# Kernel optimization log

Hardware: AMD Instinct MI355X
Metric: run time of the kernel (lower is better)

Reference implementation:

```python
import jax, jax.numpy as jnp
import numpy as np

D = 256          # input_dim
H = 4            # num_heads
W = 4            # window_size
NUM_SCALES = 3
FRACTAL = 2
NUM_CLASSES = 7


def _pool(t, ksize):
    # reflect-pad along time by ksize//2 each side, then avg_pool1d(kernel=stride=ksize)
    p = ksize // 2
    t = jnp.pad(t, ((0, 0), (p, p), (0, 0)), mode='reflect')
    B, Tp, F = t.shape
    L = Tp // ksize
    return t[:, :L * ksize].reshape(B, L, ksize, F).mean(axis=2)


def _window_attn(q, k, v):
    # windowed multi-head self-attention with zero-pad to a multiple of W
    B, T, F = q.shape
    pad = (-T) % W
    if pad:
        q = jnp.pad(q, ((0, 0), (0, pad), (0, 0)))
        k = jnp.pad(k, ((0, 0), (0, pad), (0, 0)))
        v = jnp.pad(v, ((0, 0), (0, pad), (0, 0)))
    Tp = T + pad
    nw = Tp // W
    hd = F // H
    scale = 1.0 / np.sqrt(hd).astype(np.float32)
    # [B, nw, W, H, hd] -> [B, nw, H, W, hd]
    qh = q.reshape(B, nw, W, H, hd).transpose(0, 1, 3, 2, 4)
    kh = k.reshape(B, nw, W, H, hd).transpose(0, 1, 3, 2, 4)
    vh = v.reshape(B, nw, W, H, hd).transpose(0, 1, 3, 2, 4)
    attn = jnp.einsum('bnhqd,bnhkd->bnhqk', qh, kh) * scale
    attn = jax.nn.softmax(attn, axis=-1)
    out = jnp.einsum('bnhqk,bnhkd->bnhqd', attn, vh)
    out = out.transpose(0, 1, 3, 2, 4).reshape(B, Tp, F)
    return out[:, :T]


def _upsample_nearest(f, out_len):
    # matches torch F.interpolate(mode='nearest'): src = floor(i * in / out)
    in_len = f.shape[1]
    idx = jnp.minimum((jnp.arange(out_len) * in_len) // out_len, in_len - 1)
    return f[:, idx]


def setup_inputs() -> dict:
    key = jax.random.key(0)
    ks = jax.random.split(key, 14)
    s = 1.0 / np.sqrt(D).astype(np.float32)
    inp = {
        'x': jax.random.normal(ks[0], (32, 4096, D), dtype=jnp.float32),
        'Wq': jax.random.normal(ks[1], (D, D), dtype=jnp.float32) * s,
        'bq': jnp.zeros((D,), jnp.float32),
        'Wk': jax.random.normal(ks[2], (D, D), dtype=jnp.float32) * s,
        'bk': jnp.zeros((D,), jnp.float32),
        'Wv': jax.random.normal(ks[3], (D, D), dtype=jnp.float32) * s,
        'bv': jnp.zeros((D,), jnp.float32),
        'Wp': jax.random.normal(ks[4], (D, D), dtype=jnp.float32) * s,
        'bp': jnp.zeros((D,), jnp.float32),
        'Wc1': jax.random.normal(ks[5], (D, D), dtype=jnp.float32) * s,
        'bc1': jnp.zeros((D,), jnp.float32),
        'Wc2': jax.random.normal(ks[6], (D, NUM_CLASSES), dtype=jnp.float32) * s,
        'bc2': jnp.zeros((NUM_CLASSES,), jnp.float32),
    }
    return inp


def reference(x, Wq, bq, Wk, bk, Wv, bv, Wp, bp, Wc1, bc1, Wc2, bc2):
    B, T, F = x.shape
    q = x @ Wq + bq
    k = x @ Wk + bk
    v = x @ Wv + bv
    # multi-scale temporal operator + per-scale fractal windowed attention
    outs = []
    for s_idx in range(1, NUM_SCALES + 1):
        ksize = FRACTAL ** (s_idx - 1)
        if ksize == 1:
            qs, ks_, vs = q, k, v
        else:
            qs, ks_, vs = _pool(q, ksize), _pool(k, ksize), _pool(v, ksize)
        outs.append(_window_attn(qs, ks_, vs))
    # scale mixer: nearest upsample + exact GELU + sum + proj
    summed = sum(jax.nn.gelu(_upsample_nearest(f, T), approximate=False) for f in outs)
    fused = summed @ Wp + bp
    # classifier (dropout inactive in eval)
    h = fused.mean(axis=1)
    h = jax.nn.relu(h @ Wc1 + bc1)
    logits = h @ Wc2 + bc2
    return logits
```

## Files before the change

kernel.cpp:

```cpp
#include <hip/hip_runtime.h>

#define DD 256
#define TT 4096
#define BB 32

typedef __attribute__((ext_vector_type(8))) short short8;
typedef __attribute__((ext_vector_type(4))) float floatx4;

__device__ __forceinline__ unsigned short f2bf(float f) {
    unsigned u = __builtin_bit_cast(unsigned, f);
    unsigned r = u + 0x7FFFu + ((u >> 16) & 1u);
    return (unsigned short)(r >> 16);
}
__device__ __forceinline__ float bf2f(unsigned short h) {
    return __builtin_bit_cast(float, (unsigned)h << 16);
}
__device__ __forceinline__ float2 unpk(unsigned u) {
    float2 r;
    r.x = __builtin_bit_cast(float, u << 16);
    r.y = __builtin_bit_cast(float, u & 0xFFFF0000u);
    return r;
}

#define GLDS16(g, l)                                                        \
    __builtin_amdgcn_global_load_lds(                                       \
        (const __attribute__((address_space(1))) void*)(g),                 \
        (__attribute__((address_space(3))) void*)(l), 16, 0, 0)

__global__ __launch_bounds__(256)
void prep_x_kernel(const float* __restrict__ X, unsigned short* __restrict__ Xp)
{
    size_t i = ((size_t)blockIdx.x * 256 + threadIdx.x) * 8;
    float4 a = *(const float4*)(X + i);
    float4 b = *(const float4*)(X + i + 4);
    short8 o;
    o[0] = (short)f2bf(a.x); o[1] = (short)f2bf(a.y);
    o[2] = (short)f2bf(a.z); o[3] = (short)f2bf(a.w);
    o[4] = (short)f2bf(b.x); o[5] = (short)f2bf(b.y);
    o[6] = (short)f2bf(b.z); o[7] = (short)f2bf(b.w);
    size_t row = i >> 8;
    int k = (int)(i & 255);
    size_t off = (size_t)(k >> 5) * (131072u * 32u) + row * 32 + (k & 31);
    *(short8*)(Xp + off) = o;
}

__global__ void prep_w_kernel(const float* __restrict__ Wq,
                              const float* __restrict__ Wk,
                              const float* __restrict__ Wv,
                              unsigned short* __restrict__ Wt)
{
    const int z = blockIdx.y;
    const int k = blockIdx.x;
    const int n = threadIdx.x;
    const float* W = (z == 0) ? Wq : (z == 1) ? Wk : Wv;
    float w = W[k * 256 + n];
    unsigned short hi = f2bf(w);
    unsigned short lo = f2bf(w - bf2f(hi));
    size_t base = (size_t)z * 131072;
    size_t off = (size_t)(k >> 5) * 8192 + (size_t)n * 32 + (k & 31);
    Wt[base +         off] = hi;
    Wt[base + 65536 + off] = lo;
}

__global__ __launch_bounds__(256, 3)
void qkv_mfma_kernel(const unsigned short* __restrict__ Xp,
                     const unsigned short* __restrict__ Wt,
                     const float* __restrict__ bq, const float* __restrict__ bk,
                     const float* __restrict__ bv,
                     unsigned short* __restrict__ Q, unsigned short* __restrict__ Kp,
                     unsigned short* __restrict__ V)
{
    const int z = blockIdx.z;
    const unsigned short* Wz = Wt + (size_t)z * 131072;
    const float* bias = (z == 0) ? bq : (z == 1) ? bk : bv;
    unsigned short* Y = (z == 0) ? Q : (z == 1) ? Kp : V;

    __shared__ __align__(16) unsigned char smem[49152];

    const int tid = threadIdx.x;
    const int lane = tid & 63, wave = tid >> 6;
    const int wm = wave & 1, wn = wave >> 1;
    const int l15 = lane & 15, lq = lane >> 4;
    const int col0 = blockIdx.x * 128;
    const size_t row0 = (size_t)blockIdx.y * 128;

    floatx4 acc[4][4];
    #pragma unroll
    for (int i = 0; i < 4; ++i)
        #pragma unroll
        for (int j = 0; j < 4; ++j)
            acc[i][j] = (floatx4){0.f, 0.f, 0.f, 0.f};

    auto stage = [&](int p, int pb) {
        unsigned short* As = (unsigned short*)(smem + pb * 8192);
        unsigned short* Bs = (unsigned short*)(smem + 16384 + pb * 16384);
        const unsigned short* Ap = Xp + (size_t)p * (131072u * 32u);
        const unsigned short* Bp = Wz + (size_t)p * 8192;
        #pragma unroll
        for (int it = 0; it < 2; ++it) {
            int flat = it * 256 + tid;
            int m = flat >> 2, c = flat & 3;
            int sc = c ^ ((m >> 1) & 3);
            GLDS16(Ap + (row0 + m) * 32 + sc * 8, As + flat * 8);
        }
        #pragma unroll
        for (int half = 0; half < 2; ++half)
            #pragma unroll
            for (int it = 0; it < 2; ++it) {
                int flat = it * 256 + tid;
                int n = flat >> 2, c = flat & 3;
                int sc = c ^ ((n >> 1) & 3);
                GLDS16(Bp + half * 65536 + (size_t)(col0 + n) * 32 + sc * 8,
                       Bs + half * 4096 + flat * 8);
            }
    };

    stage(0, 0);
    __syncthreads();

    for (int k = 0; k < 8; ++k) {
        const int pb = k & 1;
        if (k < 7) stage(k + 1, pb ^ 1);

        const unsigned short* As = (const unsigned short*)(smem + pb * 8192);
        const unsigned short* Bs = (const unsigned short*)(smem + 16384 + pb * 16384);

        short8 a[4];
        #pragma unroll
        for (int mt = 0; mt < 4; ++mt) {
            int row = wm * 64 + mt * 16 + l15;
            a[mt] = *(const short8*)(As + row * 32 + (lq ^ ((row >> 1) & 3)) * 8);
        }
        #pragma unroll
        for (int nt = 0; nt < 4; ++nt) {
            int nr = wn * 64 + nt * 16 + l15;
            const unsigned short* bp = Bs + nr * 32 + (lq ^ ((nr >> 1) & 3)) * 8;
            short8 bh = *(const short8*)bp;
            short8 bl = *(const short8*)(bp + 4096);
            #pragma unroll
            for (int mt = 0; mt < 4; ++mt) {
                acc[mt][nt] = __builtin_amdgcn_mfma_f32_16x16x32_bf16(a[mt], bh, acc[mt][nt], 0, 0, 0);
                acc[mt][nt] = __builtin_amdgcn_mfma_f32_16x16x32_bf16(a[mt], bl, acc[mt][nt], 0, 0, 0);
            }
        }
        __syncthreads();
    }

    unsigned short* Cs = (unsigned short*)(smem + wave * 8192);
    #pragma unroll
    for (int nt = 0; nt < 4; ++nt) {
        float bv_ = bias[col0 + wn * 64 + nt * 16 + l15];
        #pragma unroll
        for (int mt = 0; mt < 4; ++mt)
            #pragma unroll
            for (int r = 0; r < 4; ++r) {
                int row = mt * 16 + lq * 4 + r;
                Cs[row * 64 + nt * 16 + l15] = f2bf(acc[mt][nt][r] + bv_);
            }
    }
    #pragma unroll
    for (int p = 0; p < 8; ++p) {
        int row = p * 8 + (lane >> 3);
        float4 d = *(const float4*)(Cs + row * 64 + (lane & 7) * 8);
        *(float4*)(Y + (row0 + wm * 64 + row) * 256 + col0 + wn * 64 + (lane & 7) * 8) = d;
    }
}

__device__ __forceinline__ float gelu2(float x) {
    float z = fabsf(x) * 0.70710678118654752f;
    float t = __builtin_amdgcn_rcpf(fmaf(z, 0.3275911f, 1.0f));
    float p = fmaf(t, 1.061405429f, -1.453152027f);
    p = fmaf(p, t, 1.421413741f);
    p = fmaf(p, t, -0.284496736f);
    p = fmaf(p, t, 0.254829592f);
    p = p * t;
    float e = __expf(-z * z);
    float erf_abs = fmaf(-p, e, 1.0f);
    float erfv = copysignf(erf_abs, x);
    return x * (1.0f + erfv);
}
__device__ __forceinline__ void addu4(uint4 d, float* f) {
    float2 t;
    t = unpk(d.x); f[0] += t.x; f[1] += t.y;
    t = unpk(d.y); f[2] += t.x; f[3] += t.y;
    t = unpk(d.z); f[4] += t.x; f[5] += t.y;
    t = unpk(d.w); f[6] += t.x; f[7] += t.y;
}

#define SPAN 32
#define NROW 34

template<int KS>
__device__ __forceinline__ void pool_qk(const unsigned short* __restrict__ qb,
                                        const unsigned short* __restrict__ kb,
                                        int rp,
                                        float* __restrict__ qf,
                                        float* __restrict__ kf)
{
    #pragma unroll
    for (int j = 0; j < KS; ++j) {
        int ra = (rp >> (8 * j)) & 0xFF;
        uint4 qd = *(const uint4*)(qb + ra * 256);
        uint4 kd = *(const uint4*)(kb + ra * 256);
        addu4(qd, qf);
        addu4(kd, kf);
    }
}

template<int KS>
__device__ __forceinline__ void pool_v(const unsigned short* __restrict__ vb,
                                       int rp, float* __restrict__ vf)
{
    #pragma unroll
    for (int j = 0; j < KS; ++j) {
        int ra = (rp >> (8 * j)) & 0xFF;
        uint4 vd = *(const uint4*)(vb + ra * 256);
        addu4(vd, vf);
    }
}

__global__ __launch_bounds__(256, 3)
void attn_fused_kernel(const unsigned short* __restrict__ Q,
                       const unsigned short* __restrict__ K,
                       const unsigned short* __restrict__ V,
                       float* __restrict__ acc)
{
    __shared__ __align__(16) unsigned char smem[3 * NROW * 256 * 2];
    unsigned short* qkvs = (unsigned short*)smem;
    float* scratch = (float*)smem;

    const int tid = threadIdx.x;
    const int s = blockIdx.x;
    const int b = blockIdx.y;
    const int r0 = s * SPAN;
    const int rbase = r0 - 2;

    #pragma unroll
    for (int t = 0; t < 3; ++t) {
        const unsigned short* src =
            ((t == 0) ? Q : (t == 1) ? K : V) + (size_t)b * TT * DD;
        #pragma unroll
        for (int it = 0; it < 5; ++it) {
            int flat = it * 256 + tid;
            if (flat < NROW * 32) {
                int row = flat >> 5, dc = flat & 31;
                int g = rbase + row;
                g = (g < 0) ? 0 : g;
                int c = (((dc >> 2) & 3) << 3) | ((dc & 3) << 1) | ((dc >> 4) & 1);
                GLDS16(src + (size_t)g * DD + c * 8,
                       qkvs + t * (NROW * 256) + flat * 8);
            }
        }
    }
    __syncthreads();

    const int slot = tid >> 2, lq = tid & 3;
    const int head = slot & 3, u = slot >> 2;
    int ksize, LEN, w; bool active = true;
    if (u < 8)       { ksize = 1; LEN = 4096; w = s * 8 + u; }
    else if (u < 12) { ksize = 2; LEN = 2049; w = s * 4 + (u - 8); }
    else if (u < 14) { ksize = 4; LEN = 1025; w = s * 2 + (u - 12); }
    else if (u == 14){ ksize = 2; LEN = 2049; w = 512; active = (s == 127); }
    else             { ksize = 4; LEN = 1025; w = 256; active = (s == 127); }

    const int f0 = head * 64 + lq * 16;
    const int fperm = head * 32 + lq * 8;

    float accL[16];
    #pragma unroll
    for (int e = 0; e < 16; ++e) accL[e] = 0.f;

    if (active) {
        int rp[4]; float cwh[4]; int vmask = 0;
        for (int i = 0; i < 4; ++i) {
            int p = w * 4 + i;
            bool vv = (p < LEN);
            if (vv) vmask |= (1 << i);
            int pc = vv ? p : 0;
            int r[4] = {0, 0, 0, 0};
            if (ksize == 1) { r[0] = pc; }
            else if (ksize == 2) {
                if (pc == 0)            { r[0] = 0;      r[1] = 1;      }
                else if (pc == LEN - 1) { r[0] = TT - 2; r[1] = TT - 1; }
                else                    { r[0] = 2 * pc - 1; r[1] = 2 * pc; }
            } else {
                if (pc == 0)            { r[0] = 2; r[1] = 1; r[2] = 0; r[3] = 1; }
                else if (pc == LEN - 1) { r[0] = TT - 3; r[1] = TT - 2; r[2] = TT - 2; r[3] = TT - 1; }
                else                    { r[0] = 4*pc - 2; r[1] = 4*pc - 1; r[2] = 4*pc; r[3] = 4*pc + 1; }
            }
            int rr = 0;
            #pragma unroll
            for (int j = 0; j < 4; ++j) rr |= ((r[j] - rbase) & 0xFF) << (8 * j);
            rp[i] = rr;
            float c = 0.5f;
            if (ksize == 2)
                c = 0.5f * (float)(((p + 1) * TT + 2048) / 2049 - (p * TT + 2048) / 2049);
            else if (ksize == 4)
                c = 0.5f * (float)(((p + 1) * TT + 1024) / 1025 - (p * TT + 1024) / 1025);
            cwh[i] = vv ? c : 0.f;
        }
        const float inv_k = 1.0f / (float)ksize;
        const float sscale = 0.125f * inv_k * inv_k;

        float S[4][4];
        #pragma unroll
        for (int i = 0; i < 4; ++i)
            #pragma unroll
            for (int j = 0; j < 4; ++j) S[i][j] = 0.f;

        for (int half = 0; half < 2; ++half) {
            float qf[4][8], kf[4][8];
            const unsigned short* qb = qkvs + half * 128 + fperm;
            const unsigned short* kb = qb + NROW * 256;
            #pragma unroll
            for (int i = 0; i < 4; ++i) {
                #pragma unroll
                for (int e = 0; e < 8; ++e) { qf[i][e] = 0.f; kf[i][e] = 0.f; }
                if (vmask & (1 << i)) {
                    if (ksize == 1)      pool_qk<1>(qb, kb, rp[i], qf[i], kf[i]);
                    else if (ksize == 2) pool_qk<2>(qb, kb, rp[i], qf[i], kf[i]);
                    else                 pool_qk<4>(qb, kb, rp[i], qf[i], kf[i]);
                }
            }
            #pragma unroll
            for (int i = 0; i < 4; ++i)
                #pragma unroll
                for (int j = 0; j < 4; ++j) {
                    float d = 0.f;
                    #pragma unroll
                    for (int e = 0; e < 8; ++e) d = fmaf(qf[i][e], kf[j][e], d);
                    S[i][j] += d;
                }
        }
        #pragma unroll
        for (int i = 0; i < 4; ++i)
            #pragma unroll
            for (int j = 0; j < 4; ++j) {
                float t = S[i][j];
                t += __shfl_xor(t, 1, 64);
                t += __shfl_xor(t, 2, 64);
                S[i][j] = t * sscale;
            }
        float P[4][4];
        #pragma unroll
        for (int i = 0; i < 4; ++i) {
            float m = fmaxf(fmaxf(S[i][0], S[i][1]), fmaxf(S[i][2], S[i][3]));
            float e0 = __expf(S[i][0] - m), e1 = __expf(S[i][1] - m);
            float e2 = __expf(S[i][2] - m), e3 = __expf(S[i][3] - m);
            float inv = inv_k * __builtin_amdgcn_rcpf(e0 + e1 + e2 + e3);
            P[i][0] = e0 * inv; P[i][1] = e1 * inv; P[i][2] = e2 * inv; P[i][3] = e3 * inv;
        }

        for (int half = 0; half < 2; ++half) {
            float vf[4][8];
            const unsigned short* vb = qkvs + 2 * NROW * 256 + half * 128 + fperm;
            #pragma unroll
            for (int i = 0; i < 4; ++i) {
                #pragma unroll
                for (int e = 0; e < 8; ++e) vf[i][e] = 0.f;
                if (vmask & (1 << i)) {
                    if (ksize == 1)      pool_v<1>(vb, rp[i], vf[i]);
                    else if (ksize == 2) pool_v<2>(vb, rp[i], vf[i]);
                    else                 pool_v<4>(vb, rp[i], vf[i]);
                }
            }
            #pragma unroll
            for (int i = 0; i < 4; ++i) {
                if (!(vmask & (1 << i))) continue;
                #pragma unroll
                for (int e = 0; e < 8; ++e) {
                    float o = P[i][0]*vf[0][e] + P[i][1]*vf[1][e]
                            + P[i][2]*vf[2][e] + P[i][3]*vf[3][e];
                    accL[half * 8 + e] += cwh[i] * gelu2(o);
                }
            }
        }
    }

    __syncthreads();
    #pragma unroll
    for (int e = 0; e < 16; e += 4) {
        float4 d = {accL[e], accL[e+1], accL[e+2], accL[e+3]};
        *(float4*)(scratch + u * 256 + f0 + e) = d;
    }
    __syncthreads();
    float sum = 0.f;
    #pragma unroll
    for (int uu = 0; uu < 16; ++uu) sum += scratch[uu * 256 + tid];
    atomicAdd(&acc[b * DD + tid], sum);
}

__global__ __launch_bounds__(256)
void classifier_kernel(const float* __restrict__ acc,
                       const float* __restrict__ Wp,  const float* __restrict__ bp,
                       const float* __restrict__ Wc1, const float* __restrict__ bc1,
                       const float* __restrict__ Wc2, const float* __restrict__ bc2,
                       float* __restrict__ out)
{
    const int b = blockIdx.x;
    const int d = threadIdx.x;
    __shared__ float sm[256], sf[256], sh[256];

    sm[d] = acc[b * 256 + d] * (1.0f / 4096.0f);
    __syncthreads();

    float s = bp[d];
    for (int kk = 0; kk < 256; ++kk) s = fmaf(sm[kk], Wp[kk * 256 + d], s);
    sf[d] = s;
    __syncthreads();

    s = bc1[d];
    for (int kk = 0; kk < 256; ++kk) s = fmaf(sf[kk], Wc1[kk * 256 + d], s);
    sh[d] = fmaxf(s, 0.0f);
    __syncthreads();

    if (d < 7) {
        s = bc2[d];
        for (int kk = 0; kk < 256; ++kk) s = fmaf(sh[kk], Wc2[kk * 7 + d], s);
        out[b * 7 + d] = s;
    }
}

extern "C" void kernel_launch(void* const* d_in, const int* in_sizes, int n_in,
                              void* d_out, int out_size, void* d_ws, size_t ws_size,
                              hipStream_t stream)
{
    const float* x   = (const float*)d_in[0];
    const float* Wq  = (const float*)d_in[1];
    const float* bq  = (const float*)d_in[2];
    const float* Wk  = (const float*)d_in[3];
    const float* bk  = (const float*)d_in[4];
    const float* Wv  = (const float*)d_in[5];
    const float* bv  = (const float*)d_in[6];
    const float* Wp  = (const float*)d_in[7];
    const float* bp  = (const float*)d_in[8];
    const float* Wc1 = (const float*)d_in[9];
    const float* bc1 = (const float*)d_in[10];
    const float* Wc2 = (const float*)d_in[11];
    const float* bc2 = (const float*)d_in[12];
    float* out = (float*)d_out;

    const size_t plane = (size_t)BB * TT * DD;
    unsigned short* Q  = (unsigned short*)d_ws;
    unsigned short* K  = Q + plane;
    unsigned short* V  = K + plane;
    unsigned short* Xh = V + plane;
    unsigned short* Wt = Xh + plane;
    float* acc = (float*)(Wt + 3 * 131072);

    prep_x_kernel<<<dim3(16384), 256, 0, stream>>>(x, Xh);
    prep_w_kernel<<<dim3(256, 3), 256, 0, stream>>>(Wq, Wk, Wv, Wt);
    (void)hipMemsetAsync(acc, 0, BB * DD * sizeof(float), stream);

    qkv_mfma_kernel<<<dim3(2, 1024, 3), 256, 0, stream>>>(
        Xh, Wt, bq, bk, bv, Q, K, V);

    attn_fused_kernel<<<dim3(128, BB), 256, 0, stream>>>(Q, K, V, acc);

    classifier_kernel<<<dim3(BB), 256, 0, stream>>>(acc, Wp, bp, Wc1, bc1, Wc2, bc2, out);
}
```

Before: 471.7 us.

## Merge prep kernels, reorder QKV grid, specialize interior attention, shuffle reduction

```diff
diff --git a/kernel.cpp b/kernel.cpp
--- a/kernel.cpp
+++ b/kernel.cpp
@@ -28,38 +28,43 @@
         (__attribute__((address_space(3))) void*)(l), 16, 0, 0)
 
 __global__ __launch_bounds__(256)
-void prep_x_kernel(const float* __restrict__ X, unsigned short* __restrict__ Xp)
-{
-    size_t i = ((size_t)blockIdx.x * 256 + threadIdx.x) * 8;
-    float4 a = *(const float4*)(X + i);
-    float4 b = *(const float4*)(X + i + 4);
-    short8 o;
-    o[0] = (short)f2bf(a.x); o[1] = (short)f2bf(a.y);
-    o[2] = (short)f2bf(a.z); o[3] = (short)f2bf(a.w);
-    o[4] = (short)f2bf(b.x); o[5] = (short)f2bf(b.y);
-    o[6] = (short)f2bf(b.z); o[7] = (short)f2bf(b.w);
-    size_t row = i >> 8;
-    int k = (int)(i & 255);
-    size_t off = (size_t)(k >> 5) * (131072u * 32u) + row * 32 + (k & 31);
-    *(short8*)(Xp + off) = o;
-}
-
-__global__ void prep_w_kernel(const float* __restrict__ Wq,
-                              const float* __restrict__ Wk,
-                              const float* __restrict__ Wv,
-                              unsigned short* __restrict__ Wt)
-{
-    const int z = blockIdx.y;
-    const int k = blockIdx.x;
-    const int n = threadIdx.x;
-    const float* W = (z == 0) ? Wq : (z == 1) ? Wk : Wv;
-    float w = W[k * 256 + n];
-    unsigned short hi = f2bf(w);
-    unsigned short lo = f2bf(w - bf2f(hi));
-    size_t base = (size_t)z * 131072;
-    size_t off = (size_t)(k >> 5) * 8192 + (size_t)n * 32 + (k & 31);
-    Wt[base +         off] = hi;
-    Wt[base + 65536 + off] = lo;
+void prep_kernel(const float* __restrict__ X,
+                 const float* __restrict__ Wq, const float* __restrict__ Wk,
+                 const float* __restrict__ Wv,
+                 unsigned short* __restrict__ Xp, unsigned short* __restrict__ Wt,
+                 float* __restrict__ acc)
+{
+    const int bid = blockIdx.x;
+    const int tid = threadIdx.x;
+    if (bid < 16384) {
+        size_t i = ((size_t)bid * 256 + tid) * 8;
+        float4 a = *(const float4*)(X + i);
+        float4 b = *(const float4*)(X + i + 4);
+        short8 o;
+        o[0] = (short)f2bf(a.x); o[1] = (short)f2bf(a.y);
+        o[2] = (short)f2bf(a.z); o[3] = (short)f2bf(a.w);
+        o[4] = (short)f2bf(b.x); o[5] = (short)f2bf(b.y);
+        o[6] = (short)f2bf(b.z); o[7] = (short)f2bf(b.w);
+        size_t row = i >> 8;
+        int k = (int)(i & 255);
+        size_t off = (size_t)(k >> 5) * (131072u * 32u) + row * 32 + (k & 31);
+        *(short8*)(Xp + off) = o;
+    } else if (bid < 16384 + 768) {
+        const int wb = bid - 16384;
+        const int z = wb >> 8;
+        const int k = wb & 255;
+        const int n = tid;
+        const float* W = (z == 0) ? Wq : (z == 1) ? Wk : Wv;
+        float w = W[k * 256 + n];
+        unsigned short hi = f2bf(w);
+        unsigned short lo = f2bf(w - bf2f(hi));
+        size_t base = (size_t)z * 131072;
+        size_t off = (size_t)(k >> 5) * 8192 + (size_t)n * 32 + (k & 31);
+        Wt[base +         off] = hi;
+        Wt[base + 65536 + off] = lo;
+    } else {
+        for (int i = tid; i < BB * DD; i += 256) acc[i] = 0.f;
+    }
 }
 
 __global__ __launch_bounds__(256, 3)
@@ -70,7 +75,7 @@
                      unsigned short* __restrict__ Q, unsigned short* __restrict__ Kp,
                      unsigned short* __restrict__ V)
 {
-    const int z = blockIdx.z;
+    const int z = blockIdx.y;
     const unsigned short* Wz = Wt + (size_t)z * 131072;
     const float* bias = (z == 0) ? bq : (z == 1) ? bk : bv;
     unsigned short* Y = (z == 0) ? Q : (z == 1) ? Kp : V;
@@ -82,7 +87,7 @@
     const int wm = wave & 1, wn = wave >> 1;
     const int l15 = lane & 15, lq = lane >> 4;
     const int col0 = blockIdx.x * 128;
-    const size_t row0 = (size_t)blockIdx.y * 128;
+    const size_t row0 = (size_t)blockIdx.z * 128;
 
     floatx4 acc[4][4];
     #pragma unroll
@@ -219,6 +224,87 @@
     }
 }
 
+template<int KS>
+__device__ __forceinline__ void fast_unit(const unsigned short* __restrict__ qkvs,
+                                          int rowbase,
+                                          const float* __restrict__ cwh,
+                                          float sscale, float inv_k, int fperm,
+                                          float* __restrict__ accL)
+{
+    float S[4][4];
+    #pragma unroll
+    for (int i = 0; i < 4; ++i)
+        #pragma unroll
+        for (int j = 0; j < 4; ++j) S[i][j] = 0.f;
+
+    #pragma unroll
+    for (int half = 0; half < 2; ++half) {
+        const unsigned short* qb = qkvs + half * 128 + fperm + rowbase * 256;
+        const unsigned short* kb = qb + NROW * 256;
+        float qf[4][8], kf[4][8];
+        #pragma unroll
+        for (int i = 0; i < 4; ++i) {
+            #pragma unroll
+            for (int e = 0; e < 8; ++e) { qf[i][e] = 0.f; kf[i][e] = 0.f; }
+            #pragma unroll
+            for (int j = 0; j < KS; ++j) {
+                addu4(*(const uint4*)(qb + (i * KS + j) * 256), qf[i]);
+                addu4(*(const uint4*)(kb + (i * KS + j) * 256), kf[i]);
+            }
+        }
+        #pragma unroll
+        for (int i = 0; i < 4; ++i)
+            #pragma unroll
+            for (int j = 0; j < 4; ++j) {
+                float d = 0.f;
+                #pragma unroll
+                for (int e = 0; e < 8; ++e) d = fmaf(qf[i][e], kf[j][e], d);
+                S[i][j] += d;
+            }
+    }
+    #pragma unroll
+    for (int i = 0; i < 4; ++i)
+        #pragma unroll
+        for (int j = 0; j < 4; ++j) {
+            float t = S[i][j];
+            t += __shfl_xor(t, 1, 64);
+            t += __shfl_xor(t, 2, 64);
+            S[i][j] = t * sscale;
+        }
+    float P[4][4];
+    #pragma unroll
+    for (int i = 0; i < 4; ++i) {
+        float m = fmaxf(fmaxf(S[i][0], S[i][1]), fmaxf(S[i][2], S[i][3]));
+        float e0 = __expf(S[i][0] - m), e1 = __expf(S[i][1] - m);
+        float e2 = __expf(S[i][2] - m), e3 = __expf(S[i][3] - m);
+        float inv = inv_k * __builtin_amdgcn_rcpf(e0 + e1 + e2 + e3);
+        P[i][0] = e0 * inv; P[i][1] = e1 * inv; P[i][2] = e2 * inv; P[i][3] = e3 * inv;
+    }
+    #pragma unroll
+    for (int half = 0; half < 2; ++half) {
+        const unsigned short* vb =
+            qkvs + 2 * NROW * 256 + half * 128 + fperm + rowbase * 256;
+        float vf[4][8];
+        #pragma unroll
+        for (int i = 0; i < 4; ++i) {
+            #pragma unroll
+            for (int e = 0; e < 8; ++e) vf[i][e] = 0.f;
+            #pragma unroll
+            for (int j = 0; j < KS; ++j)
+                addu4(*(const uint4*)(vb + (i * KS + j) * 256), vf[i]);
+        }
+        #pragma unroll
+        for (int i = 0; i < 4; ++i) {
+            #pragma unroll
+            for (int e = 0; e < 8; ++e) {
+                float o = P[i][0]*vf[0][e] + P[i][1]*vf[1][e]
+                        + P[i][2]*vf[2][e] + P[i][3]*vf[3][e];
+                accL[half * 8 + e] += cwh[i] * gelu2(o);
+            }
+        }
+    }
+}
+
 __global__ __launch_bounds__(256, 3)
 void attn_fused_kernel(const unsigned short* __restrict__ Q,
                        const unsigned short* __restrict__ K,
@@ -227,7 +313,6 @@
 {
     __shared__ __align__(16) unsigned char smem[3 * NROW * 256 * 2];
     unsigned short* qkvs = (unsigned short*)smem;
-    float* scratch = (float*)smem;
 
     const int tid = threadIdx.x;
     const int s = blockIdx.x;
@@ -270,7 +355,34 @@
     #pragma unroll
     for (int e = 0; e < 16; ++e) accL[e] = 0.f;
 
-    if (active) {
+    const bool generic = (s == 0) || (s == 127);
+
+    if (!generic) {
+        if (active) {
+            float cwh[4];
+            if (ksize == 1) {
+                #pragma unroll
+                for (int i = 0; i < 4; ++i) cwh[i] = 0.5f;
+                fast_unit<1>(qkvs, u * 4 + 2, cwh, 0.125f, 1.0f, fperm, accL);
+            } else if (ksize == 2) {
+                #pragma unroll
+                for (int i = 0; i < 4; ++i) {
+                    int p = 16 * s + 4 * (u - 8) + i;
+                    cwh[i] = 0.5f * (float)(((p + 1) * TT + 2048) / 2049
+                                          - (p * TT + 2048) / 2049);
+                }
+                fast_unit<2>(qkvs, 8 * (u - 8) + 1, cwh, 0.03125f, 0.5f, fperm, accL);
+            } else {
+                #pragma unroll
+                for (int i = 0; i < 4; ++i) {
+                    int p = 8 * s + 4 * (u - 12) + i;
+                    cwh[i] = 0.5f * (float)(((p + 1) * TT + 1024) / 1025
+                                          - (p * TT + 1024) / 1025);
+                }
+                fast_unit<4>(qkvs, 16 * (u - 12), cwh, 0.0078125f, 0.25f, fperm, accL);
+            }
+        }
+    } else if (active) {
         int rp[4]; float cwh[4]; int vmask = 0;
         for (int i = 0; i < 4; ++i) {
             int p = w * 4 + i;
@@ -350,7 +462,6 @@
             float inv = inv_k * __builtin_amdgcn_rcpf(e0 + e1 + e2 + e3);
             P[i][0] = e0 * inv; P[i][1] = e1 * inv; P[i][2] = e2 * inv; P[i][3] = e3 * inv;
         }
-
         for (int half = 0; half < 2; ++half) {
             float vf[4][8];
             const unsigned short* vb = qkvs + 2 * NROW * 256 + half * 128 + fperm;
@@ -377,17 +488,18 @@
         }
     }
 
-    __syncthreads();
-    #pragma unroll
-    for (int e = 0; e < 16; e += 4) {
-        float4 d = {accL[e], accL[e+1], accL[e+2], accL[e+3]};
-        *(float4*)(scratch + u * 256 + f0 + e) = d;
-    }
-    __syncthreads();
-    float sum = 0.f;
-    #pragma unroll
-    for (int uu = 0; uu < 16; ++uu) sum += scratch[uu * 256 + tid];
-    atomicAdd(&acc[b * DD + tid], sum);
+    #pragma unroll
+    for (int e = 0; e < 16; ++e) {
+        float t = accL[e];
+        t += __shfl_xor(t, 16, 64);
+        t += __shfl_xor(t, 32, 64);
+        accL[e] = t;
+    }
+    if ((tid & 48) == 0) {
+        #pragma unroll
+        for (int e = 0; e < 16; ++e)
+            atomicAdd(&acc[b * DD + f0 + e], accL[e]);
+    }
 }
 
 __global__ __launch_bounds__(256)
@@ -448,11 +560,10 @@
     unsigned short* Wt = Xh + plane;
     float* acc = (float*)(Wt + 3 * 131072);
 
-    prep_x_kernel<<<dim3(16384), 256, 0, stream>>>(x, Xh);
-    prep_w_kernel<<<dim3(256, 3), 256, 0, stream>>>(Wq, Wk, Wv, Wt);
-    (void)hipMemsetAsync(acc, 0, BB * DD * sizeof(float), stream);
-
-    qkv_mfma_kernel<<<dim3(2, 1024, 3), 256, 0, stream>>>(
+    prep_kernel<<<dim3(16384 + 768 + 1), 256, 0, stream>>>(
+        x, Wq, Wk, Wv, Xh, Wt, acc);
+
+    qkv_mfma_kernel<<<dim3(2, 3, 1024), 256, 0, stream>>>(
         Xh, Wt, bq, bk, bv, Q, K, V);
 
     attn_fused_kernel<<<dim3(128, BB), 256, 0, stream>>>(Q, K, V, acc);
```

New measurement: 1.067 ms. +126.2%, slower.
